# Performance work log

Hardware: AMD Instinct MI355X
Metric: run time of the kernel (lower is better)

Reference implementation:

```python
import jax, jax.numpy as jnp
import numpy as np

B, N, D = 4, 2048, 1024
H = 16
HD = D // H  # head_dim = 64
SCALE = HD ** -0.5


def setup_inputs() -> dict:
    key = jax.random.key(0)
    k1, k2, k3, k4 = jax.random.split(key, 4)
    x = jax.random.normal(k1, (B, N, D), dtype=jnp.float32)
    # init-scale weights for numerically sane softmax logits
    w_qkv = jax.random.normal(k2, (3 * D, D), dtype=jnp.float32) * 0.02
    w_proj = jax.random.normal(k3, (D, D), dtype=jnp.float32) * 0.02
    b_proj = jax.random.normal(k4, (D,), dtype=jnp.float32) * 0.02
    return {"x": x, "w_qkv": w_qkv, "w_proj": w_proj, "b_proj": b_proj}


def reference(x, w_qkv, w_proj, b_proj):
    # qkv projection (width_mult=1.0 -> Dyna slicing is identity; qkv_bias=False)
    qkv = jnp.einsum('bnd,ed->bne', x, w_qkv)          # (B, N, 3D)
    qkv = qkv.reshape(B, N, 3, H, HD)
    q = qkv[:, :, 0].transpose(0, 2, 1, 3)              # (B, H, N, HD)
    k = qkv[:, :, 1].transpose(0, 2, 1, 3)
    v = qkv[:, :, 2].transpose(0, 2, 1, 3)
    q = q * SCALE
    attn = jnp.einsum('bhqd,bhkd->bhqk', q, k)          # (B, H, N, N)
    attn = jax.nn.softmax(attn, axis=-1)
    out = jnp.einsum('bhqk,bhkd->bhqd', attn, v)        # (B, H, N, HD)
    out = out.transpose(0, 2, 1, 3).reshape(B, N, D)
    # output projection (bias=True)
    return jnp.einsum('bnd,ed->bne', out, w_proj) + b_proj
```

## Files before the change

### kernel.cpp

```cpp
#include <hip/hip_runtime.h>
#include <hip/hip_bf16.h>
#include <stdint.h>


typedef __attribute__((ext_vector_type(8))) short short8;
typedef __attribute__((ext_vector_type(4))) short short4v;
typedef __attribute__((ext_vector_type(4))) float float4v;

#define MFMA16(a, b, c) __builtin_amdgcn_mfma_f32_16x16x32_bf16((a), (b), (c), 0, 0, 0)
#define MFMA16K16(a, b, c) __builtin_amdgcn_mfma_f32_16x16x16bf16_1k((a), (b), (c), 0, 0, 0)

static __device__ __forceinline__ unsigned short f2bf(float f) {
  union { float f; unsigned u; } v; v.f = f;
  unsigned r = v.u + 0x7fffu + ((v.u >> 16) & 1u);
  return (unsigned short)(r >> 16);
}
static __device__ __forceinline__ float bf2f(unsigned short u) {
  union { unsigned u; float f; } v; v.u = ((unsigned)u) << 16;
  return v.f;
}
static __device__ __forceinline__ unsigned pkbf(float a, float b) {
  union { __hip_bfloat162 v; unsigned u; } c;
  c.v = __float22bfloat162_rn(make_float2(a, b));
  return c.u;
}
static __device__ __forceinline__ float ex2(float x) {
#if __has_builtin(__builtin_amdgcn_exp2f)
  return __builtin_amdgcn_exp2f(x);
#else
  return exp2f(x);
#endif
}
static __device__ __forceinline__ float4v fzero() {
  float4v z; z[0] = 0.f; z[1] = 0.f; z[2] = 0.f; z[3] = 0.f; return z;
}
static __device__ __forceinline__ void load_lds16(const void* g, void* l) {
  typedef const __attribute__((address_space(1))) void* gp_t;
  typedef __attribute__((address_space(3))) void* lp_t;
  __builtin_amdgcn_global_load_lds((gp_t)(uintptr_t)g, (lp_t)(uint32_t)(uintptr_t)l, 16, 0, 0);
}

__global__ void detect_dtype(const unsigned short* __restrict__ x, int* flag) {
  __shared__ int cnt;
  if (threadIdx.x == 0) cnt = 0;
  __syncthreads();
  int c = 0;
  for (int i = threadIdx.x; i < 4096; i += 256) {
    const unsigned v = x[i] & 0x7FFFu;
    if ((v >> 7) >= 134u) ++c;
  }
  atomicAdd(&cnt, c);
  __syncthreads();
  if (threadIdx.x == 0) *flag = (cnt > 64) ? 1 : 0;
}

static __device__ __forceinline__ void cv8(const void* src, unsigned short* dst,
                                           int i, int fl) {
  if (fl) {
    const float4v a = *(const float4v*)((const float*)src + i);
    const float4v b = *(const float4v*)((const float*)src + i + 4);
    short8 o;
    o[0] = (short)f2bf(a[0]); o[1] = (short)f2bf(a[1]);
    o[2] = (short)f2bf(a[2]); o[3] = (short)f2bf(a[3]);
    o[4] = (short)f2bf(b[0]); o[5] = (short)f2bf(b[1]);
    o[6] = (short)f2bf(b[2]); o[7] = (short)f2bf(b[3]);
    *(short8*)(dst + i) = o;
  } else {
    *(short8*)(dst + i) = *(const short8*)((const unsigned short*)src + i);
  }
}
__global__ __launch_bounds__(256) void convert_all(
    const void* __restrict__ s0, const void* __restrict__ s1,
    const void* __restrict__ s2, const void* __restrict__ s3,
    unsigned short* __restrict__ d0, unsigned short* __restrict__ d1,
    unsigned short* __restrict__ d2, unsigned short* __restrict__ d3,
    const int* __restrict__ flag) {
  const int t = blockIdx.x * 256 + threadIdx.x;
  const int fl = *flag;
  if (t < 1048576)       cv8(s0, d0, t * 8, fl);
  else if (t < 1441792)  cv8(s1, d1, (t - 1048576) * 8, fl);
  else if (t < 1572864)  cv8(s2, d2, (t - 1441792) * 8, fl);
  else if (t < 1572992)  cv8(s3, d3, (t - 1572864) * 8, fl);
}

__global__ __launch_bounds__(256) void qkv_gemm(
    const unsigned short* __restrict__ X, const unsigned short* __restrict__ W,
    unsigned short* __restrict__ Qo, unsigned short* __restrict__ Ko,
    unsigned short* __restrict__ Vt) {
  __shared__ __attribute__((aligned(16))) unsigned short lA[2][128 * 32];
  __shared__ __attribute__((aligned(16))) unsigned short lB[2][128 * 32];
  const int tid = threadIdx.x;
  const int wave = tid >> 6, lane = tid & 63, quad = lane >> 4, l16 = lane & 15;
  const int wm = wave >> 1, wn = wave & 1;
  const int m0 = blockIdx.x * 128, n0 = blockIdx.y * 128;

  float4v acc[4][4];
  for (int i = 0; i < 4; ++i) for (int j = 0; j < 4; ++j) acc[i][j] = fzero();

  const int f0 = tid, f1 = 256 + tid;
  const int r0 = f0 >> 2, c0 = (f0 & 3) * 8;
  const int r1 = f1 >> 2, c1 = (f1 & 3) * 8;
  const int dof0 = (wave * 64) * 8;
  const int dof1 = (256 + wave * 64) * 8;

#define QKV_STAGE(buf, k0)                                                   \
  load_lds16(X + (size_t)(m0 + r0) * 1024 + (k0) + c0, lA[buf] + dof0);      \
  load_lds16(X + (size_t)(m0 + r1) * 1024 + (k0) + c1, lA[buf] + dof1);      \
  load_lds16(W + (size_t)(n0 + r0) * 1024 + (k0) + c0, lB[buf] + dof0);      \
  load_lds16(W + (size_t)(n0 + r1) * 1024 + (k0) + c1, lB[buf] + dof1);

  QKV_STAGE(0, 0);
  __syncthreads();
  int cur = 0;
  for (int k0 = 0; k0 < 1024; k0 += 32) {
    if (k0 < 992) { QKV_STAGE(cur ^ 1, k0 + 32); }
    short8 af[4], bfr[4];
    for (int t = 0; t < 4; ++t) {
      af[t]  = *(const short8*)(lA[cur] + (wm * 64 + t * 16 + l16) * 32 + quad * 8);
      bfr[t] = *(const short8*)(lB[cur] + (wn * 64 + t * 16 + l16) * 32 + quad * 8);
    }
    for (int mt = 0; mt < 4; ++mt)
      for (int nt = 0; nt < 4; ++nt)
        acc[mt][nt] = MFMA16(af[mt], bfr[nt], acc[mt][nt]);
    __syncthreads();
    cur ^= 1;
  }
#undef QKV_STAGE

  const float QSCALE = 0.18033688011112042f;
  for (int mt = 0; mt < 4; ++mt) {
    const int mbase = m0 + wm * 64 + mt * 16 + quad * 4;
    const int b = mbase >> 11;
    const int nrow = mbase & 2047;
    for (int nt = 0; nt < 4; ++nt) {
      const int e = n0 + wn * 64 + nt * 16 + l16;
      const int c = e >> 10, h = (e >> 6) & 15, hd = e & 63;
      const int bh = b * 16 + h;
      if (c == 0) {
        for (int r = 0; r < 4; ++r)
          Qo[((size_t)bh * 2048 + nrow + r) * 64 + hd] = f2bf(acc[mt][nt][r] * QSCALE);
      } else if (c == 1) {
        for (int r = 0; r < 4; ++r)
          Ko[((size_t)bh * 2048 + nrow + r) * 64 + hd] = f2bf(acc[mt][nt][r]);
      } else {
        short4v pk;
        for (int r = 0; r < 4; ++r) pk[r] = (short)f2bf(acc[mt][nt][r]);
        *(short4v*)(Vt + ((size_t)bh * 64 + hd) * 2048 + nrow) = pk;
      }
    }
  }
}

__global__ __launch_bounds__(256, 4) void flash_attn(
    const unsigned short* __restrict__ Q, const unsigned short* __restrict__ K,
    const unsigned short* __restrict__ Vt, unsigned short* __restrict__ AO) {
  __shared__ __attribute__((aligned(16))) unsigned short lK[2][64 * 72];
  __shared__ __attribute__((aligned(16))) unsigned short lV[2][64 * 72];
  const int tid = threadIdx.x;
  const int wave = tid >> 6, lane = tid & 63, quad = lane >> 4, l16 = lane & 15;
  const int qt = blockIdx.x, bh = blockIdx.y;
  const int b = bh >> 4, h = bh & 15;
  const size_t base = (size_t)bh * 2048 * 64;
  const unsigned short* Qp = Q + base;
  const unsigned short* Kp = K + base;
  const unsigned short* Vp = Vt + base;
  const int q0 = qt * 128;

  const int qa = q0 + wave * 16 + l16;
  const short8 qfA0 = *(const short8*)(Qp + (size_t)qa * 64 + quad * 8);
  const short8 qfA1 = *(const short8*)(Qp + (size_t)qa * 64 + 32 + quad * 8);
  const short8 qfB0 = *(const short8*)(Qp + (size_t)(qa + 64) * 64 + quad * 8);
  const short8 qfB1 = *(const short8*)(Qp + (size_t)(qa + 64) * 64 + 32 + quad * 8);

  float4v oaccA[4], oaccB[4];
  for (int i = 0; i < 4; ++i) { oaccA[i] = fzero(); oaccB[i] = fzero(); }
  float lsumA = 0.f, lsumB = 0.f;

  const int f0 = tid, f1 = 256 + tid;
  const int sk0 = (f0 >> 3) * 72 + (f0 & 7) * 8;
  const int sk1 = (f1 >> 3) * 72 + (f1 & 7) * 8;

  short8 kv0 = *(const short8*)(Kp + f0 * 8);
  short8 kv1 = *(const short8*)(Kp + f1 * 8);
  short8 vv0 = *(const short8*)(Vp + (size_t)(f0 >> 3) * 2048 + (f0 & 7) * 8);
  short8 vv1 = *(const short8*)(Vp + (size_t)(f1 >> 3) * 2048 + (f1 & 7) * 8);

  for (int kb = 0; kb < 32; ++kb) {
    unsigned short* const Kb = lK[kb & 1];
    unsigned short* const Vb = lV[kb & 1];
    *(short8*)(Kb + sk0) = kv0;
    *(short8*)(Kb + sk1) = kv1;
    *(short8*)(Vb + sk0) = vv0;
    *(short8*)(Vb + sk1) = vv1;
    __syncthreads();
    if (kb < 31) {
      const size_t ko = (size_t)(kb + 1) * 4096;
      kv0 = *(const short8*)(Kp + ko + f0 * 8);
      kv1 = *(const short8*)(Kp + ko + f1 * 8);
      vv0 = *(const short8*)(Vp + (size_t)(f0 >> 3) * 2048 + (kb + 1) * 64 + (f0 & 7) * 8);
      vv1 = *(const short8*)(Vp + (size_t)(f1 >> 3) * 2048 + (kb + 1) * 64 + (f1 & 7) * 8);
    }

#pragma unroll
    for (int t = 0; t < 4; ++t) {
      const short8 k0f = *(const short8*)(Kb + (t * 16 + l16) * 72 + quad * 8);
      const short8 k1f = *(const short8*)(Kb + (t * 16 + l16) * 72 + 32 + quad * 8);
      float4v sA = MFMA16(k0f, qfA0, fzero());
      sA = MFMA16(k1f, qfA1, sA);
      float4v sB = MFMA16(k0f, qfB0, fzero());
      sB = MFMA16(k1f, qfB1, sB);

      const float eA0 = ex2(sA[0]), eA1 = ex2(sA[1]);
      const float eA2 = ex2(sA[2]), eA3 = ex2(sA[3]);
      const float eB0 = ex2(sB[0]), eB1 = ex2(sB[1]);
      const float eB2 = ex2(sB[2]), eB3 = ex2(sB[3]);
      lsumA += (eA0 + eA1) + (eA2 + eA3);
      lsumB += (eB0 + eB1) + (eB2 + eB3);
      union { unsigned u[2]; short4v s; } ca, cb;
      ca.u[0] = pkbf(eA0, eA1); ca.u[1] = pkbf(eA2, eA3);
      cb.u[0] = pkbf(eB0, eB1); cb.u[1] = pkbf(eB2, eB3);

      const unsigned short* vrow = Vb + l16 * 72 + quad * 4 + t * 16;
#pragma unroll
      for (int nt = 0; nt < 4; ++nt) {
        const short4v vf = *(const short4v*)(vrow + nt * 16 * 72);
        oaccA[nt] = MFMA16K16(vf, ca.s, oaccA[nt]);
        oaccB[nt] = MFMA16K16(vf, cb.s, oaccB[nt]);
      }
    }
  }

  lsumA += __shfl_xor(lsumA, 16); lsumA += __shfl_xor(lsumA, 32);
  lsumB += __shfl_xor(lsumB, 16); lsumB += __shfl_xor(lsumB, 32);
  const float invA = 1.f / lsumA, invB = 1.f / lsumB;

  unsigned short* aoA = AO + ((size_t)(b * 2048 + qa)) * 1024 + h * 64 + quad * 4;
  unsigned short* aoB = aoA + (size_t)64 * 1024;
  for (int nt = 0; nt < 4; ++nt) {
    union { unsigned u[2]; short4v s; } oa, ob;
    oa.u[0] = pkbf(oaccA[nt][0] * invA, oaccA[nt][1] * invA);
    oa.u[1] = pkbf(oaccA[nt][2] * invA, oaccA[nt][3] * invA);
    ob.u[0] = pkbf(oaccB[nt][0] * invB, oaccB[nt][1] * invB);
    ob.u[1] = pkbf(oaccB[nt][2] * invB, oaccB[nt][3] * invB);
    *(short4v*)(aoA + nt * 16) = oa.s;
    *(short4v*)(aoB + nt * 16) = ob.s;
  }
}

__global__ __launch_bounds__(256) void proj_gemm(
    const unsigned short* __restrict__ A, const unsigned short* __restrict__ W,
    const unsigned short* __restrict__ bias_bf, const void* __restrict__ bias_raw,
    void* __restrict__ outv, const int* __restrict__ flag) {
  __shared__ __attribute__((aligned(16))) unsigned short lA[2][128 * 32];
  __shared__ __attribute__((aligned(16))) unsigned short lB[2][128 * 32];
  const int tid = threadIdx.x;
  const int wave = tid >> 6, lane = tid & 63, quad = lane >> 4, l16 = lane & 15;
  const int wm = wave >> 1, wn = wave & 1;
  const int m0 = blockIdx.x * 128, n0 = blockIdx.y * 128;
  const int fl = *flag;

  float4v acc[4][4];
  for (int i = 0; i < 4; ++i) for (int j = 0; j < 4; ++j) acc[i][j] = fzero();

  const int f0 = tid, f1 = 256 + tid;
  const int r0 = f0 >> 2, c0 = (f0 & 3) * 8;
  const int r1 = f1 >> 2, c1 = (f1 & 3) * 8;
  const int dof0 = (wave * 64) * 8;
  const int dof1 = (256 + wave * 64) * 8;

#define PROJ_STAGE(buf, k0)                                                  \
  load_lds16(A + (size_t)(m0 + r0) * 1024 + (k0) + c0, lA[buf] + dof0);      \
  load_lds16(A + (size_t)(m0 + r1) * 1024 + (k0) + c1, lA[buf] + dof1);     \
  load_lds16(W + (size_t)(n0 + r0) * 1024 + (k0) + c0, lB[buf] + dof0);      \
  load_lds16(W + (size_t)(n0 + r1) * 1024 + (k0) + c1, lB[buf] + dof1);

  PROJ_STAGE(0, 0);
  __syncthreads();
  int cur = 0;
  for (int k0 = 0; k0 < 1024; k0 += 32) {
    if (k0 < 992) { PROJ_STAGE(cur ^ 1, k0 + 32); }
    short8 af[4], bfr[4];
    for (int t = 0; t < 4; ++t) {
      af[t]  = *(const short8*)(lA[cur] + (wm * 64 + t * 16 + l16) * 32 + quad * 8);
      bfr[t] = *(const short8*)(lB[cur] + (wn * 64 + t * 16 + l16) * 32 + quad * 8);
    }
    for (int mt = 0; mt < 4; ++mt)
      for (int nt = 0; nt < 4; ++nt)
        acc[mt][nt] = MFMA16(af[mt], bfr[nt], acc[mt][nt]);
    __syncthreads();
    cur ^= 1;
  }
#undef PROJ_STAGE

  for (int mt = 0; mt < 4; ++mt) {
    const int mbase = m0 + wm * 64 + mt * 16 + quad * 4;
    for (int nt = 0; nt < 4; ++nt) {
      const int e = n0 + wn * 64 + nt * 16 + l16;
      const float bv = fl ? ((const float*)bias_raw)[e] : bf2f(bias_bf[e]);
      for (int r = 0; r < 4; ++r) {
        const float val = acc[mt][nt][r] + bv;
        const size_t idx = (size_t)(mbase + r) * 1024 + e;
        if (fl) ((float*)outv)[idx] = val;
        else    ((unsigned short*)outv)[idx] = f2bf(val);
      }
    }
  }
}

extern "C" void kernel_launch(void* const* d_in, const int* in_sizes, int n_in,
                              void* d_out, int out_size, void* d_ws, size_t ws_size,
                              hipStream_t stream) {
  const void* x_raw     = d_in[0];
  const void* wqkv_raw  = d_in[1];
  const void* wproj_raw = d_in[2];
  const void* bproj_raw = d_in[3];

  const size_t NE = (size_t)4 * 16 * 2048 * 64;
  unsigned short* ws = (unsigned short*)d_ws;
  unsigned short* Q      = ws;
  unsigned short* K      = Q + NE;
  unsigned short* Vt     = K + NE;
  unsigned short* xb     = Vt + NE;
  unsigned short* AO     = xb;
  unsigned short* wqkvb  = xb + NE;
  unsigned short* wprojb = wqkvb + 3145728;
  unsigned short* bprojb = wprojb + 1048576;
  int* flag = (int*)(bprojb + 1024);

  detect_dtype<<<1, 256, 0, stream>>>((const unsigned short*)x_raw, flag);
  convert_all<<<6145, 256, 0, stream>>>(x_raw, wqkv_raw, wproj_raw, bproj_raw,
                                        xb, wqkvb, wprojb, bprojb, flag);

  qkv_gemm<<<dim3(64, 24), 256, 0, stream>>>(xb, wqkvb, Q, K, Vt);
  flash_attn<<<dim3(16, 64), 256, 0, stream>>>(Q, K, Vt, AO);
  proj_gemm<<<dim3(64, 8), 256, 0, stream>>>(AO, wprojb, bprojb, bproj_raw,
                                             d_out, flag);
}
```

Measured before the change: 271.2 us.

## Switch flash attention inner loop to 32x32x16 MFMA with permlane fragment shuffle

The attention kernel now computes QK^T and PV with 32x32x16 bf16 MFMA tiles instead of 16x16 tiles. Each wave owns 32 query rows. The exp'd probabilities are rearranged into the B-operand layout with v_permlane32_swap rather than relying on the 16x16x16 K16 instruction for PV. The aim is fewer MFMA issues, larger per-instruction work and fewer LDS fragment reads, at the cost of a 16-wide accumulator register footprint and a layout shuffle.

```diff
diff --git a/kernel.cpp b/kernel.cpp
--- a/kernel.cpp
+++ b/kernel.cpp
@@ -6,9 +6,10 @@
 typedef __attribute__((ext_vector_type(8))) short short8;
 typedef __attribute__((ext_vector_type(4))) short short4v;
 typedef __attribute__((ext_vector_type(4))) float float4v;
+typedef __attribute__((ext_vector_type(16))) float float16v;
 
 #define MFMA16(a, b, c) __builtin_amdgcn_mfma_f32_16x16x32_bf16((a), (b), (c), 0, 0, 0)
-#define MFMA16K16(a, b, c) __builtin_amdgcn_mfma_f32_16x16x16bf16_1k((a), (b), (c), 0, 0, 0)
+#define MFMA32(a, b, c) __builtin_amdgcn_mfma_f32_32x32x16_bf16((a), (b), (c), 0, 0, 0)
 
 static __device__ __forceinline__ unsigned short f2bf(float f) {
   union { float f; unsigned u; } v; v.f = f;
@@ -33,6 +34,15 @@
 }
 static __device__ __forceinline__ float4v fzero() {
   float4v z; z[0] = 0.f; z[1] = 0.f; z[2] = 0.f; z[3] = 0.f; return z;
+}
+static __device__ __forceinline__ float16v fzero16() {
+  float16v z;
+#pragma unroll
+  for (int i = 0; i < 16; ++i) z[i] = 0.f;
+  return z;
+}
+static __device__ __forceinline__ void pl32swap(unsigned& a, unsigned& b) {
+  asm volatile("v_permlane32_swap_b32 %0, %1" : "+v"(a), "+v"(b));
 }
 static __device__ __forceinline__ void load_lds16(const void* g, void* l) {
   typedef const __attribute__((address_space(1))) void* gp_t;
@@ -157,7 +167,8 @@
   __shared__ __attribute__((aligned(16))) unsigned short lK[2][64 * 72];
   __shared__ __attribute__((aligned(16))) unsigned short lV[2][64 * 72];
   const int tid = threadIdx.x;
-  const int wave = tid >> 6, lane = tid & 63, quad = lane >> 4, l16 = lane & 15;
+  const int wave = tid >> 6, lane = tid & 63;
+  const int l31 = lane & 31, hi = lane >> 5;
   const int qt = blockIdx.x, bh = blockIdx.y;
   const int b = bh >> 4, h = bh & 15;
   const size_t base = (size_t)bh * 2048 * 64;
@@ -166,15 +177,14 @@
   const unsigned short* Vp = Vt + base;
   const int q0 = qt * 128;
 
-  const int qa = q0 + wave * 16 + l16;
-  const short8 qfA0 = *(const short8*)(Qp + (size_t)qa * 64 + quad * 8);
-  const short8 qfA1 = *(const short8*)(Qp + (size_t)qa * 64 + 32 + quad * 8);
-  const short8 qfB0 = *(const short8*)(Qp + (size_t)(qa + 64) * 64 + quad * 8);
-  const short8 qfB1 = *(const short8*)(Qp + (size_t)(qa + 64) * 64 + 32 + quad * 8);
-
-  float4v oaccA[4], oaccB[4];
-  for (int i = 0; i < 4; ++i) { oaccA[i] = fzero(); oaccB[i] = fzero(); }
-  float lsumA = 0.f, lsumB = 0.f;
+  const int qa = q0 + wave * 32 + l31;
+  short8 qf[4];
+#pragma unroll
+  for (int j = 0; j < 4; ++j)
+    qf[j] = *(const short8*)(Qp + (size_t)qa * 64 + j * 16 + hi * 8);
+
+  float16v oacc0 = fzero16(), oacc1 = fzero16();
+  float lsum = 0.f;
 
   const int f0 = tid, f1 = 256 + tid;
   const int sk0 = (f0 >> 3) * 72 + (f0 & 7) * 8;
@@ -202,48 +212,53 @@
     }
 
 #pragma unroll
-    for (int t = 0; t < 4; ++t) {
-      const short8 k0f = *(const short8*)(Kb + (t * 16 + l16) * 72 + quad * 8);
-      const short8 k1f = *(const short8*)(Kb + (t * 16 + l16) * 72 + 32 + quad * 8);
-      float4v sA = MFMA16(k0f, qfA0, fzero());
-      sA = MFMA16(k1f, qfA1, sA);
-      float4v sB = MFMA16(k0f, qfB0, fzero());
-      sB = MFMA16(k1f, qfB1, sB);
-
-      const float eA0 = ex2(sA[0]), eA1 = ex2(sA[1]);
-      const float eA2 = ex2(sA[2]), eA3 = ex2(sA[3]);
-      const float eB0 = ex2(sB[0]), eB1 = ex2(sB[1]);
-      const float eB2 = ex2(sB[2]), eB3 = ex2(sB[3]);
-      lsumA += (eA0 + eA1) + (eA2 + eA3);
-      lsumB += (eB0 + eB1) + (eB2 + eB3);
-      union { unsigned u[2]; short4v s; } ca, cb;
-      ca.u[0] = pkbf(eA0, eA1); ca.u[1] = pkbf(eA2, eA3);
-      cb.u[0] = pkbf(eB0, eB1); cb.u[1] = pkbf(eB2, eB3);
-
-      const unsigned short* vrow = Vb + l16 * 72 + quad * 4 + t * 16;
-#pragma unroll
-      for (int nt = 0; nt < 4; ++nt) {
-        const short4v vf = *(const short4v*)(vrow + nt * 16 * 72);
-        oaccA[nt] = MFMA16K16(vf, ca.s, oaccA[nt]);
-        oaccB[nt] = MFMA16K16(vf, cb.s, oaccB[nt]);
+    for (int kb2 = 0; kb2 < 2; ++kb2) {
+      const unsigned short* krow = Kb + (kb2 * 32 + l31) * 72 + hi * 8;
+      float16v s = fzero16();
+#pragma unroll
+      for (int j = 0; j < 4; ++j)
+        s = MFMA32(*(const short8*)(krow + j * 16), qf[j], s);
+
+      unsigned u[8];
+      float ls = 0.f;
+#pragma unroll
+      for (int j = 0; j < 8; ++j) {
+        const float e0 = ex2(s[2 * j]);
+        const float e1 = ex2(s[2 * j + 1]);
+        ls += e0 + e1;
+        u[j] = pkbf(e0, e1);
       }
-    }
-  }
-
-  lsumA += __shfl_xor(lsumA, 16); lsumA += __shfl_xor(lsumA, 32);
-  lsumB += __shfl_xor(lsumB, 16); lsumB += __shfl_xor(lsumB, 32);
-  const float invA = 1.f / lsumA, invB = 1.f / lsumB;
-
-  unsigned short* aoA = AO + ((size_t)(b * 2048 + qa)) * 1024 + h * 64 + quad * 4;
-  unsigned short* aoB = aoA + (size_t)64 * 1024;
-  for (int nt = 0; nt < 4; ++nt) {
-    union { unsigned u[2]; short4v s; } oa, ob;
-    oa.u[0] = pkbf(oaccA[nt][0] * invA, oaccA[nt][1] * invA);
-    oa.u[1] = pkbf(oaccA[nt][2] * invA, oaccA[nt][3] * invA);
-    ob.u[0] = pkbf(oaccB[nt][0] * invB, oaccB[nt][1] * invB);
-    ob.u[1] = pkbf(oaccB[nt][2] * invB, oaccB[nt][3] * invB);
-    *(short4v*)(aoA + nt * 16) = oa.s;
-    *(short4v*)(aoB + nt * 16) = ob.s;
+      lsum += ls;
+
+      pl32swap(u[0], u[2]); pl32swap(u[1], u[3]);
+      pl32swap(u[4], u[6]); pl32swap(u[5], u[7]);
+      union { unsigned w[4]; short8 s8; } fr0, fr1;
+      fr0.w[0] = u[0]; fr0.w[1] = u[1]; fr0.w[2] = u[2]; fr0.w[3] = u[3];
+      fr1.w[0] = u[4]; fr1.w[1] = u[5]; fr1.w[2] = u[6]; fr1.w[3] = u[7];
+
+      const unsigned short* vrow0 = Vb + l31 * 72 + kb2 * 32 + hi * 8;
+      const unsigned short* vrow1 = vrow0 + 32 * 72;
+      oacc0 = MFMA32(*(const short8*)(vrow0), fr0.s8, oacc0);
+      oacc1 = MFMA32(*(const short8*)(vrow1), fr0.s8, oacc1);
+      oacc0 = MFMA32(*(const short8*)(vrow0 + 16), fr1.s8, oacc0);
+      oacc1 = MFMA32(*(const short8*)(vrow1 + 16), fr1.s8, oacc1);
+    }
+  }
+
+  lsum += __shfl_xor(lsum, 32);
+  const float inv = 1.f / lsum;
+
+  unsigned short* ao = AO + ((size_t)(b * 2048 + qa)) * 1024 + h * 64 + hi * 4;
+#pragma unroll
+  for (int mt = 0; mt < 2; ++mt) {
+    const float16v& oc = mt ? oacc1 : oacc0;
+#pragma unroll
+    for (int g = 0; g < 4; ++g) {
+      union { unsigned u2[2]; short4v s4; } o;
+      o.u2[0] = pkbf(oc[4 * g] * inv, oc[4 * g + 1] * inv);
+      o.u2[1] = pkbf(oc[4 * g + 2] * inv, oc[4 * g + 3] * inv);
+      *(short4v*)(ao + mt * 32 + g * 8) = o.s4;
+    }
   }
 }
 
```

New measurement: 279.1 us. 2.9% more time.
